# Kernel optimization log

Hardware: AMD Instinct MI355X
Metric: run time of the kernel (lower is better)

Reference implementation:

```python
import jax, jax.numpy as jnp
import numpy as np

B, DIM, L, S, E = 4096, 3, 300, 60, 128
P = L // S  # points per local region = 5


def setup_inputs() -> dict:
    key = jax.random.key(0)
    ks = jax.random.split(key, 9)
    inp = {
        "x": jax.random.normal(ks[0], (B, DIM, L), dtype=jnp.float32),
        # local_emb_nn: Conv1d(DIM, E, 1) -> weight [E, DIM], bias [E]
        "W_le": jax.random.normal(ks[1], (E, DIM), dtype=jnp.float32) * 0.1,
        "b_le": jax.random.normal(ks[2], (E,), dtype=jnp.float32) * 0.1,
        "W_lr": jax.random.normal(ks[3], (S, P), dtype=jnp.float32) * 0.1,
        "b_lr": jax.random.normal(ks[4], (S,), dtype=jnp.float32) * 0.1,
        # global_emb_nn: Conv1d(DIM, E, 1)
        "W_ge": jax.random.normal(ks[5], (E, DIM), dtype=jnp.float32) * 0.1,
        "b_ge": jax.random.normal(ks[6], (E,), dtype=jnp.float32) * 0.1,
        # global_nn: Conv1d(L, 1, 1) -> weight [L], bias scalar
        "W_gn": jax.random.normal(ks[7], (L,), dtype=jnp.float32) * 0.1,
        "b_gn": jax.random.normal(ks[8], (), dtype=jnp.float32) * 0.1,
    }
    return inp


def reference(x, W_le, b_le, W_lr, b_lr, W_ge, b_ge, W_gn, b_gn):
    # global branch: [B,DIM,L] -> [B,E,L] -> relu -> transpose [B,L,E]
    gf = jax.nn.relu(jnp.einsum('ec,bcl->ble', W_ge, x) + b_ge)
    # global_nn: 1x1 conv over L channels -> [B,E], then relu
    gf = jax.nn.relu(jnp.einsum('l,ble->be', W_gn, gf) + b_gn)
    # local branch: [B,DIM,L] -> [B,E,L] -> relu -> transpose [B,L,E]
    lf = jax.nn.relu(jnp.einsum('ec,bcl->ble', W_le, x) + b_le)
    # chunk into S regions of P points, apply per-region 1x1 conv (P->1)
    lf = lf.reshape(B, S, P, E)
    lf = jnp.einsum('sp,bspe->bse', W_lr, lf) + b_lr[None, :, None]
    # add broadcast global feature [B,1,E]
    return lf + gf[:, None, :]
```

## Files before the change

kernel.cpp:

```cpp
#include <hip/hip_runtime.h>


#define RELU(v) fmaxf((v), 0.0f)

__global__ __launch_bounds__(64) void cle_kernel(
    const float* __restrict__ x,
    const float* __restrict__ W_le,
    const float* __restrict__ b_le,
    const float* __restrict__ W_lr,
    const float* __restrict__ b_lr,
    const float* __restrict__ W_ge,
    const float* __restrict__ b_ge,
    const float* __restrict__ W_gn,
    const float* __restrict__ b_gn,
    float* __restrict__ out)
{
    const int lane = threadIdx.x;
    const int b = blockIdx.x;
    const int e0 = lane << 1;

    __shared__ __align__(16) float4 sx4[225];

    {
        const float4* xg4 = (const float4*)(x + (size_t)b * 900);
        sx4[lane]       = xg4[lane];
        sx4[lane + 64]  = xg4[lane + 64];
        sx4[lane + 128] = xg4[lane + 128];
        if (lane < 33) sx4[lane + 192] = xg4[lane + 192];
    }

    const float wg00 = W_ge[e0 * 3 + 0], wg01 = W_ge[e0 * 3 + 1], wg02 = W_ge[e0 * 3 + 2];
    const float wg10 = W_ge[e0 * 3 + 3], wg11 = W_ge[e0 * 3 + 4], wg12 = W_ge[e0 * 3 + 5];
    const float bg0 = b_ge[e0], bg1 = b_ge[e0 + 1];
    const float bgn = b_gn[0];

    __syncthreads();

    float ga0 = 0.f, ga1 = 0.f, ga2 = 0.f, ga3 = 0.f;
    float gb0 = 0.f, gb1 = 0.f, gb2 = 0.f, gb3 = 0.f;
#define GE0(cmp) RELU(fmaf(wg02, c2.cmp, fmaf(wg01, c1.cmp, fmaf(wg00, c0.cmp, bg0))))
#define GE1(cmp) RELU(fmaf(wg12, c2.cmp, fmaf(wg11, c1.cmp, fmaf(wg10, c0.cmp, bg1))))
    for (int g = 0; g < 15; ++g) {
        const int q0 = g * 5;
#pragma unroll
        for (int qi = 0; qi < 5; ++qi) {
            const int qq = q0 + qi;
            const int l4 = qq * 4;
            const float4 c0 = sx4[qq], c1 = sx4[75 + qq], c2 = sx4[150 + qq];
            ga0 = fmaf(W_gn[l4 + 0], GE0(x), ga0);
            gb0 = fmaf(W_gn[l4 + 0], GE1(x), gb0);
            ga1 = fmaf(W_gn[l4 + 1], GE0(y), ga1);
            gb1 = fmaf(W_gn[l4 + 1], GE1(y), gb1);
            ga2 = fmaf(W_gn[l4 + 2], GE0(z), ga2);
            gb2 = fmaf(W_gn[l4 + 2], GE1(z), gb2);
            ga3 = fmaf(W_gn[l4 + 3], GE0(w), ga3);
            gb3 = fmaf(W_gn[l4 + 3], GE1(w), gb3);
        }
    }
    const float gf0 = RELU(((ga0 + ga1) + (ga2 + ga3)) + bgn);
    const float gf1 = RELU(((gb0 + gb1) + (gb2 + gb3)) + bgn);

    const float wl00 = W_le[e0 * 3 + 0], wl01 = W_le[e0 * 3 + 1], wl02 = W_le[e0 * 3 + 2];
    const float wl10 = W_le[e0 * 3 + 3], wl11 = W_le[e0 * 3 + 4], wl12 = W_le[e0 * 3 + 5];
    const float bl0 = b_le[e0], bl1 = b_le[e0 + 1];

    float2* ob2 = (float2*)(out + (size_t)b * (60 * 128)) + lane;

#define LE0(cmp) RELU(fmaf(wl02, c2.cmp, fmaf(wl01, c1.cmp, fmaf(wl00, c0.cmp, bl0))))
#define LE1(cmp) RELU(fmaf(wl12, c2.cmp, fmaf(wl11, c1.cmp, fmaf(wl10, c0.cmp, bl1))))
#define DOQ(qi, R0, R1, R2, R3)                                                \
    {                                                                          \
        const int qq = q0 + (qi);                                              \
        const int lw = qq * 4;                 \
        const float4 c0 = sx4[qq], c1 = sx4[75 + qq], c2 = sx4[150 + qq];      \
        a0##R0 = fmaf(W_lr[lw + 0], LE0(x), a0##R0);                           \
        a1##R0 = fmaf(W_lr[lw + 0], LE1(x), a1##R0);                           \
        a0##R1 = fmaf(W_lr[lw + 1], LE0(y), a0##R1);                           \
        a1##R1 = fmaf(W_lr[lw + 1], LE1(y), a1##R1);                           \
        a0##R2 = fmaf(W_lr[lw + 2], LE0(z), a0##R2);                           \
        a1##R2 = fmaf(W_lr[lw + 2], LE1(z), a1##R2);                           \
        a0##R3 = fmaf(W_lr[lw + 3], LE0(w), a0##R3);                           \
        a1##R3 = fmaf(W_lr[lw + 3], LE1(w), a1##R3);                           \
    }

    for (int g = 0; g < 15; ++g) {
        const int q0 = g * 5;
        float a00 = 0.f, a01 = 0.f, a02 = 0.f, a03 = 0.f;
        float a10 = 0.f, a11 = 0.f, a12 = 0.f, a13 = 0.f;
        DOQ(0, 0, 0, 0, 0)
        DOQ(1, 0, 1, 1, 1)
        DOQ(2, 1, 1, 2, 2)
        DOQ(3, 2, 2, 2, 3)
        DOQ(4, 3, 3, 3, 3)

        const int s0 = g * 4;
        ob2[(s0 + 0) * 64] = make_float2(a00 + gf0 + b_lr[s0 + 0], a10 + gf1 + b_lr[s0 + 0]);
        ob2[(s0 + 1) * 64] = make_float2(a01 + gf0 + b_lr[s0 + 1], a11 + gf1 + b_lr[s0 + 1]);
        ob2[(s0 + 2) * 64] = make_float2(a02 + gf0 + b_lr[s0 + 2], a12 + gf1 + b_lr[s0 + 2]);
        ob2[(s0 + 3) * 64] = make_float2(a03 + gf0 + b_lr[s0 + 3], a13 + gf1 + b_lr[s0 + 3]);
    }
}

extern "C" void kernel_launch(void* const* d_in, const int* in_sizes, int n_in,
                              void* d_out, int out_size, void* d_ws, size_t ws_size,
                              hipStream_t stream) {
    const float* x    = (const float*)d_in[0];
    const float* W_le = (const float*)d_in[1];
    const float* b_le = (const float*)d_in[2];
    const float* W_lr = (const float*)d_in[3];
    const float* b_lr = (const float*)d_in[4];
    const float* W_ge = (const float*)d_in[5];
    const float* b_ge = (const float*)d_in[6];
    const float* W_gn = (const float*)d_in[7];
    const float* b_gn = (const float*)d_in[8];
    float* out = (float*)d_out;

    cle_kernel<<<4096, 64, 0, stream>>>(x, W_le, b_le, W_lr, b_lr,
                                        W_ge, b_ge, W_gn, b_gn, out);
}
```

Before: 46.52 us.

## Split per-batch work across four waves with shared-memory reduction of global feature

Each block now uses 256 threads. Four waves each handle a quarter of the points for the global reduction and a quarter of the local regions. Partial global sums are combined through shared memory after a barrier. This shortens the serial per-wave dependency chain and spreads output stores across more waves, at the cost of an extra barrier and uneven wave work.

```diff
diff --git a/kernel.cpp b/kernel.cpp
--- a/kernel.cpp
+++ b/kernel.cpp
@@ -3,7 +3,7 @@
 
 #define RELU(v) fmaxf((v), 0.0f)
 
-__global__ __launch_bounds__(64) void cle_kernel(
+__global__ __launch_bounds__(256) void cle_kernel(
     const float* __restrict__ x,
     const float* __restrict__ W_le,
     const float* __restrict__ b_le,
@@ -15,23 +15,23 @@
     const float* __restrict__ b_gn,
     float* __restrict__ out)
 {
-    const int lane = threadIdx.x;
-    const int b = blockIdx.x;
-    const int e0 = lane << 1;
+    const int tid  = threadIdx.x;
+    const int lane = tid & 63;
+    const int wq   = __builtin_amdgcn_readfirstlane(tid >> 6);
+    const int b    = blockIdx.x;
+    const int e0   = lane << 1;
 
     __shared__ __align__(16) float4 sx4[225];
+    __shared__ float2 sgp[4][64];
 
-    {
-        const float4* xg4 = (const float4*)(x + (size_t)b * 900);
-        sx4[lane]       = xg4[lane];
-        sx4[lane + 64]  = xg4[lane + 64];
-        sx4[lane + 128] = xg4[lane + 128];
-        if (lane < 33) sx4[lane + 192] = xg4[lane + 192];
-    }
+    if (tid < 225) sx4[tid] = ((const float4*)(x + (size_t)b * 900))[tid];
 
     const float wg00 = W_ge[e0 * 3 + 0], wg01 = W_ge[e0 * 3 + 1], wg02 = W_ge[e0 * 3 + 2];
     const float wg10 = W_ge[e0 * 3 + 3], wg11 = W_ge[e0 * 3 + 4], wg12 = W_ge[e0 * 3 + 5];
     const float bg0 = b_ge[e0], bg1 = b_ge[e0 + 1];
+    const float wl00 = W_le[e0 * 3 + 0], wl01 = W_le[e0 * 3 + 1], wl02 = W_le[e0 * 3 + 2];
+    const float wl10 = W_le[e0 * 3 + 3], wl11 = W_le[e0 * 3 + 4], wl12 = W_le[e0 * 3 + 5];
+    const float bl0 = b_le[e0], bl1 = b_le[e0 + 1];
     const float bgn = b_gn[0];
 
     __syncthreads();
@@ -40,29 +40,38 @@
     float gb0 = 0.f, gb1 = 0.f, gb2 = 0.f, gb3 = 0.f;
 #define GE0(cmp) RELU(fmaf(wg02, c2.cmp, fmaf(wg01, c1.cmp, fmaf(wg00, c0.cmp, bg0))))
 #define GE1(cmp) RELU(fmaf(wg12, c2.cmp, fmaf(wg11, c1.cmp, fmaf(wg10, c0.cmp, bg1))))
-    for (int g = 0; g < 15; ++g) {
-        const int q0 = g * 5;
+    {
+        const int qb = wq * 20;
+        const int nq = (wq < 3) ? 20 : 15;
+        for (int g = 0; g < 4; ++g) {
+            if (g * 5 < nq) {
 #pragma unroll
-        for (int qi = 0; qi < 5; ++qi) {
-            const int qq = q0 + qi;
-            const int l4 = qq * 4;
-            const float4 c0 = sx4[qq], c1 = sx4[75 + qq], c2 = sx4[150 + qq];
-            ga0 = fmaf(W_gn[l4 + 0], GE0(x), ga0);
-            gb0 = fmaf(W_gn[l4 + 0], GE1(x), gb0);
-            ga1 = fmaf(W_gn[l4 + 1], GE0(y), ga1);
-            gb1 = fmaf(W_gn[l4 + 1], GE1(y), gb1);
-            ga2 = fmaf(W_gn[l4 + 2], GE0(z), ga2);
-            gb2 = fmaf(W_gn[l4 + 2], GE1(z), gb2);
-            ga3 = fmaf(W_gn[l4 + 3], GE0(w), ga3);
-            gb3 = fmaf(W_gn[l4 + 3], GE1(w), gb3);
+                for (int qi = 0; qi < 5; ++qi) {
+                    const int qq = qb + g * 5 + qi;
+                    const int l4 = qq * 4;
+                    const float4 c0 = sx4[qq], c1 = sx4[75 + qq], c2 = sx4[150 + qq];
+                    ga0 = fmaf(W_gn[l4 + 0], GE0(x), ga0);
+                    gb0 = fmaf(W_gn[l4 + 0], GE1(x), gb0);
+                    ga1 = fmaf(W_gn[l4 + 1], GE0(y), ga1);
+                    gb1 = fmaf(W_gn[l4 + 1], GE1(y), gb1);
+                    ga2 = fmaf(W_gn[l4 + 2], GE0(z), ga2);
+                    gb2 = fmaf(W_gn[l4 + 2], GE1(z), gb2);
+                    ga3 = fmaf(W_gn[l4 + 3], GE0(w), ga3);
+                    gb3 = fmaf(W_gn[l4 + 3], GE1(w), gb3);
+                }
+            }
         }
     }
-    const float gf0 = RELU(((ga0 + ga1) + (ga2 + ga3)) + bgn);
-    const float gf1 = RELU(((gb0 + gb1) + (gb2 + gb3)) + bgn);
+    sgp[wq][lane] = make_float2((ga0 + ga1) + (ga2 + ga3), (gb0 + gb1) + (gb2 + gb3));
+    __syncthreads();
 
-    const float wl00 = W_le[e0 * 3 + 0], wl01 = W_le[e0 * 3 + 1], wl02 = W_le[e0 * 3 + 2];
-    const float wl10 = W_le[e0 * 3 + 3], wl11 = W_le[e0 * 3 + 4], wl12 = W_le[e0 * 3 + 5];
-    const float bl0 = b_le[e0], bl1 = b_le[e0 + 1];
+    float gf0, gf1;
+    {
+        const float2 p0 = sgp[0][lane], p1 = sgp[1][lane];
+        const float2 p2 = sgp[2][lane], p3 = sgp[3][lane];
+        gf0 = RELU(((p0.x + p1.x) + (p2.x + p3.x)) + bgn);
+        gf1 = RELU(((p0.y + p1.y) + (p2.y + p3.y)) + bgn);
+    }
 
     float2* ob2 = (float2*)(out + (size_t)b * (60 * 128)) + lane;
 
@@ -83,21 +92,26 @@
         a1##R3 = fmaf(W_lr[lw + 3], LE1(w), a1##R3);                           \
     }
 
-    for (int g = 0; g < 15; ++g) {
-        const int q0 = g * 5;
-        float a00 = 0.f, a01 = 0.f, a02 = 0.f, a03 = 0.f;
-        float a10 = 0.f, a11 = 0.f, a12 = 0.f, a13 = 0.f;
-        DOQ(0, 0, 0, 0, 0)
-        DOQ(1, 0, 1, 1, 1)
-        DOQ(2, 1, 1, 2, 2)
-        DOQ(3, 2, 2, 2, 3)
-        DOQ(4, 3, 3, 3, 3)
+    {
+        const int ng = (wq < 3) ? 4 : 3;
+        for (int g = 0; g < 4; ++g) {
+            if (g < ng) {
+                const int q0 = wq * 20 + g * 5;
+                float a00 = 0.f, a01 = 0.f, a02 = 0.f, a03 = 0.f;
+                float a10 = 0.f, a11 = 0.f, a12 = 0.f, a13 = 0.f;
+                DOQ(0, 0, 0, 0, 0)
+                DOQ(1, 0, 1, 1, 1)
+                DOQ(2, 1, 1, 2, 2)
+                DOQ(3, 2, 2, 2, 3)
+                DOQ(4, 3, 3, 3, 3)
 
-        const int s0 = g * 4;
-        ob2[(s0 + 0) * 64] = make_float2(a00 + gf0 + b_lr[s0 + 0], a10 + gf1 + b_lr[s0 + 0]);
-        ob2[(s0 + 1) * 64] = make_float2(a01 + gf0 + b_lr[s0 + 1], a11 + gf1 + b_lr[s0 + 1]);
-        ob2[(s0 + 2) * 64] = make_float2(a02 + gf0 + b_lr[s0 + 2], a12 + gf1 + b_lr[s0 + 2]);
-        ob2[(s0 + 3) * 64] = make_float2(a03 + gf0 + b_lr[s0 + 3], a13 + gf1 + b_lr[s0 + 3]);
+                const int s0 = wq * 16 + g * 4;
+                ob2[(s0 + 0) * 64] = make_float2(a00 + gf0 + b_lr[s0 + 0], a10 + gf1 + b_lr[s0 + 0]);
+                ob2[(s0 + 1) * 64] = make_float2(a01 + gf0 + b_lr[s0 + 1], a11 + gf1 + b_lr[s0 + 1]);
+                ob2[(s0 + 2) * 64] = make_float2(a02 + gf0 + b_lr[s0 + 2], a12 + gf1 + b_lr[s0 + 2]);
+                ob2[(s0 + 3) * 64] = make_float2(a03 + gf0 + b_lr[s0 + 3], a13 + gf1 + b_lr[s0 + 3]);
+            }
+        }
     }
 }
 
@@ -115,6 +129,6 @@
     const float* b_gn = (const float*)d_in[8];
     float* out = (float*)d_out;
 
-    cle_kernel<<<4096, 64, 0, stream>>>(x, W_le, b_le, W_lr, b_lr,
-                                        W_ge, b_ge, W_gn, b_gn, out);
+    cle_kernel<<<4096, 256, 0, stream>>>(x, W_le, b_le, W_lr, b_lr,
+                                         W_ge, b_ge, W_gn, b_gn, out);
 }
```

Result: faster. 45.60 us (-2.0%).
